# Kernel tuning notes

Hardware: AMD Instinct MI355X
Metric: run time of the kernel (lower is better)

## Reference

```python
import jax, jax.numpy as jnp
import numpy as np

N = 4000      # number_of_sensors
D_IN = 128    # input feature dim
D_OUT = 128   # output feature dim
E_DIM = 16    # node embedding dim
B = 8         # batch size


def setup_inputs() -> dict:
    key = jax.random.key(0)
    k_x, k_e1, k_e2, k_w = jax.random.split(key, 4)
    x = jax.random.normal(k_x, (B, N, D_IN), dtype=jnp.float32)
    E1 = jax.random.normal(k_e1, (N, E_DIM), dtype=jnp.float32)
    E2 = jax.random.normal(k_e2, (N, E_DIM), dtype=jnp.float32)
    W = jax.random.normal(k_w, (D_IN, D_OUT), dtype=jnp.float32) * (1.0 / np.sqrt(D_IN))
    b = jnp.zeros((D_OUT,), dtype=jnp.float32)
    return {"x": x, "E1": E1, "E2": E2, "W": W, "b": b}


def reference(x, E1, E2, W, b):
    # Adaptive adjacency from node embeddings: A = softmax(relu(E1 @ E2^T), axis=-1)
    logits = jax.nn.relu(jnp.einsum('nd,md->nm', E1, E2))  # [N, N]
    adj = jax.nn.softmax(logits, axis=-1)                  # row-normalized adjacency
    # Graph aggregation then feature transform: relu(A @ X @ W + b)
    agg = jnp.einsum('nm,bmf->bnf', adj, x)                # [B, N, D_IN]
    out = jax.nn.relu(jnp.einsum('bnf,fo->bno', agg, W) + b)  # [B, N, D_OUT]
    return out
```

## Files before the change

kernel.cpp:

```cpp
#include <hip/hip_runtime.h>
#include <hip/hip_bf16.h>

#define NSEN 4000
#define NP   4096
#define DIN  128
#define DOUT 128
#define EDIM 16
#define BATCH 8

typedef __attribute__((ext_vector_type(8))) short bf16x8;
typedef __attribute__((ext_vector_type(4))) float f32x4;

__device__ __forceinline__ unsigned short f2bf(float f) {
  unsigned int u = __float_as_uint(f);
  unsigned int r = (u + 0x7FFFu + ((u >> 16) & 1u)) >> 16;
  return (unsigned short)r;
}
__device__ __forceinline__ float bf2f(unsigned short s) {
  unsigned int u = ((unsigned int)s) << 16;
  return __uint_as_float(u);
}

__device__ __forceinline__ void gl_lds16(const void* g, void* l) {
  __builtin_amdgcn_global_load_lds((const __attribute__((address_space(1))) void*)g,
                                   (__attribute__((address_space(3))) void*)l, 16, 0, 0);
}

__global__ __launch_bounds__(512) void k_prep(const float* __restrict__ E1,
                                              const float* __restrict__ E2,
                                              const float* __restrict__ W,
                                              const float* __restrict__ x,
                                              unsigned short* __restrict__ adjp,
                                              float* __restrict__ rinv,
                                              unsigned short* __restrict__ Wt,
                                              unsigned short* __restrict__ xpt) {
  __shared__ float rsum[8][16];
  __shared__ unsigned short xtile[2][64][72];
  const int bx = blockIdx.x;
  const int tid = threadIdx.x;

  if (bx == 250) {
    for (int i = tid; i < DIN * DOUT; i += 512) {
      int o = i >> 7, f = i & 127;
      Wt[i] = f2bf(W[(size_t)f * DOUT + o]);
    }
    return;
  }
  if (bx > 250) {
    const int tile = (bx - 251) * 2 + (tid >> 8);
    const int t = tid & 255;
    const int sub = tid >> 8;
    const int m0 = (tile & 63) * 64;
    const int f0 = ((tile >> 6) & 1) * 64;
    const int b  = tile >> 7;
    const int f4 = t & 15, mrow = t >> 4;
#pragma unroll
    for (int rep = 0; rep < 4; rep++) {
      int ml = mrow + rep * 16;
      int m = m0 + ml;
      float4 v = make_float4(0.f, 0.f, 0.f, 0.f);
      if (m < NSEN) v = *(const float4*)&x[((size_t)b * NSEN + m) * DIN + f0 + f4 * 4];
      xtile[sub][f4*4+0][ml] = f2bf(v.x);
      xtile[sub][f4*4+1][ml] = f2bf(v.y);
      xtile[sub][f4*4+2][ml] = f2bf(v.z);
      xtile[sub][f4*4+3][ml] = f2bf(v.w);
    }
    __syncthreads();
    const int seg = t & 7, fl0 = t >> 3;
#pragma unroll
    for (int it = 0; it < 2; it++) {
      int fl = fl0 + it * 32;
      int j = b * DIN + f0 + fl;
      uint4 v = *(const uint4*)&xtile[sub][fl][seg * 8];
      *(uint4*)&xpt[(size_t)j * NP + m0 + seg * 8] = v;
    }
    return;
  }

  const int lane = tid & 63, wv = tid >> 6;
  const int lr = lane & 15, lq = lane >> 4;
  const int n0 = bx * 16;

  float a[8];
  {
    const float* e1p = &E1[(size_t)(n0 + lr) * EDIM + (lq & 1) * 8];
    *(float4*)&a[0] = *(const float4*)e1p;
    *(float4*)&a[4] = *(const float4*)(e1p + 4);
  }
  bf16x8 af1, af2;
#pragma unroll
  for (int j = 0; j < 8; j++) {
    unsigned short hs = f2bf(a[j]);
    af1[j] = (short)hs;
    float lo = a[j] - bf2f(hs);
    af2[j] = (lq < 2) ? (short)f2bf(lo) : (short)0;
  }

  float rs[4] = {0.f, 0.f, 0.f, 0.f};
  for (int t = wv; t < NSEN / 16; t += 8) {
    const int m = t * 16 + lr;
    float bv[8];
    const float* e2p = &E2[(size_t)m * EDIM + (lq & 1) * 8];
    *(float4*)&bv[0] = *(const float4*)e2p;
    *(float4*)&bv[4] = *(const float4*)(e2p + 4);
    bf16x8 bfrag;
#pragma unroll
    for (int j = 0; j < 8; j++) {
      unsigned short hs = f2bf(bv[j]);
      if (lq < 2) bfrag[j] = (short)hs;
      else        bfrag[j] = (short)f2bf(bv[j] - bf2f(hs));
    }
    f32x4 c = (f32x4){0.f, 0.f, 0.f, 0.f};
    c = __builtin_amdgcn_mfma_f32_16x16x32_bf16(af1, bfrag, c, 0, 0, 0);
    c = __builtin_amdgcn_mfma_f32_16x16x32_bf16(af2, bfrag, c, 0, 0, 0);
#pragma unroll
    for (int i = 0; i < 4; i++) {
      float p = __expf(fmaxf(c[i], 0.f));
      rs[i] += p;
      adjp[(size_t)(n0 + lq * 4 + i) * NP + t * 16 + lr] = f2bf(p);
    }
  }
  for (int i = tid; i < 16 * (NP - NSEN); i += 512) {
    int r = i / (NP - NSEN), c = i % (NP - NSEN);
    adjp[(size_t)(n0 + r) * NP + NSEN + c] = 0;
  }
#pragma unroll
  for (int i = 0; i < 4; i++) {
    rs[i] += __shfl_xor(rs[i], 1, 64);
    rs[i] += __shfl_xor(rs[i], 2, 64);
    rs[i] += __shfl_xor(rs[i], 4, 64);
    rs[i] += __shfl_xor(rs[i], 8, 64);
  }
  if (lr == 0) {
#pragma unroll
    for (int i = 0; i < 4; i++) rsum[wv][lq * 4 + i] = rs[i];
  }
  __syncthreads();
  if (tid < 16) {
    float s = 0.f;
#pragma unroll
    for (int w = 0; w < 8; w++) s += rsum[w][tid];
    rinv[n0 + tid] = 1.0f / s;
  }
}

__global__ __launch_bounds__(256, 2) void k_gemm1(const unsigned short* __restrict__ A,
                                                  const unsigned short* __restrict__ Bt,
                                                  unsigned short* __restrict__ part) {
  __shared__ __align__(16) unsigned short smem[32768];
  const int tid = threadIdx.x;
  const int lane = tid & 63, wv = tid >> 6;
  const int wr = wv >> 1, wc = wv & 1;
  const int lr = lane & 15, lq = lane >> 4;
  const int gx = blockIdx.x;
  const int m0 = (gx >> 1) * 128;
  const int kb0 = (gx & 1) * 2048;
  const int b  = blockIdx.y;
  const int c0 = b * 128;
  unsigned short* tA0 = smem;
  unsigned short* tB0 = smem + 16384;

  f32x4 acc[4][4];
#pragma unroll
  for (int p = 0; p < 4; p++)
#pragma unroll
    for (int q = 0; q < 4; q++) acc[p][q] = (f32x4){0.f, 0.f, 0.f, 0.f};

#define STAGE(bufi, kb)                                                              \
  {                                                                                  \
    _Pragma("unroll")                                                                \
    for (int s = 0; s < 4; s++) {                                                    \
      int idx = s * 256 + tid;                                                       \
      int row = idx >> 3;                                                            \
      int kc = ((idx & 7) ^ (row & 7)) << 3;                                         \
      gl_lds16(&A[(size_t)(m0 + row) * NP + (kb) + kc], &tA0[(bufi)*8192 + idx*8]);  \
      gl_lds16(&Bt[(size_t)(c0 + row) * NP + (kb) + kc], &tB0[(bufi)*8192 + idx*8]); \
    }                                                                                \
  }

  STAGE(0, kb0);

  for (int it = 0; it < 32; ++it) {
    const int cur = it & 1;
    if (it < 31) {
      STAGE(cur ^ 1, kb0 + (it + 1) * 64);
      asm volatile("s_waitcnt vmcnt(8)" ::: "memory");
    } else {
      asm volatile("s_waitcnt vmcnt(0)" ::: "memory");
    }
    __builtin_amdgcn_s_barrier();

    bf16x8 af0[4], bf0[4], af1[4], bf1[4];
    {
      const int koff0 = (lq * 8) ^ ((lr & 7) << 3);
#pragma unroll
      for (int p = 0; p < 4; p++)
        af0[p] = *(const bf16x8*)&tA0[cur * 8192 + (wr * 64 + p * 16 + lr) * 64 + koff0];
#pragma unroll
      for (int q = 0; q < 4; q++)
        bf0[q] = *(const bf16x8*)&tB0[cur * 8192 + (wc * 64 + q * 16 + lr) * 64 + koff0];
    }
    __builtin_amdgcn_sched_barrier(0);
    {
      const int koff1 = (32 + lq * 8) ^ ((lr & 7) << 3);
#pragma unroll
      for (int p = 0; p < 4; p++)
        af1[p] = *(const bf16x8*)&tA0[cur * 8192 + (wr * 64 + p * 16 + lr) * 64 + koff1];
#pragma unroll
      for (int q = 0; q < 4; q++)
        bf1[q] = *(const bf16x8*)&tB0[cur * 8192 + (wc * 64 + q * 16 + lr) * 64 + koff1];
    }
    asm volatile("s_waitcnt lgkmcnt(8)" ::: "memory");
    __builtin_amdgcn_sched_barrier(0);
    __builtin_amdgcn_s_setprio(1);
#pragma unroll
    for (int p = 0; p < 4; p++)
#pragma unroll
      for (int q = 0; q < 4; q++)
        acc[p][q] = __builtin_amdgcn_mfma_f32_16x16x32_bf16(af0[p], bf0[q], acc[p][q], 0, 0, 0);
    asm volatile("s_waitcnt lgkmcnt(0)" ::: "memory");
    __builtin_amdgcn_sched_barrier(0);
#pragma unroll
    for (int p = 0; p < 4; p++)
#pragma unroll
      for (int q = 0; q < 4; q++)
        acc[p][q] = __builtin_amdgcn_mfma_f32_16x16x32_bf16(af1[p], bf1[q], acc[p][q], 0, 0, 0);
    __builtin_amdgcn_s_setprio(0);
    __builtin_amdgcn_s_barrier();
  }
#undef STAGE

  const int kh = gx & 1;
  unsigned short* pdst = part + ((size_t)(kh * BATCH + b) * NP + m0) * DIN;
#pragma unroll
  for (int p = 0; p < 4; p++)
#pragma unroll
    for (int q = 0; q < 4; q++) {
      const int col = wc * 64 + q * 16 + lr;
#pragma unroll
      for (int i = 0; i < 4; i++) {
        const int row = wr * 64 + p * 16 + lq * 4 + i;
        pdst[row * DIN + col] = f2bf(acc[p][q][i]);
      }
    }
}

__global__ __launch_bounds__(256, 2) void k_fin(const unsigned short* __restrict__ part,
                                                const unsigned short* __restrict__ Wt,
                                                const float* __restrict__ rinv,
                                                const float* __restrict__ bias,
                                                float* __restrict__ out) {
  __shared__ __align__(16) unsigned short eps[64 * 136];
  const int tid = threadIdx.x;
  const int lane = tid & 63, wv = tid >> 6;
  const int wr = wv >> 1, wc = wv & 1;
  const int lr = lane & 15, lq = lane >> 4;
  const int m0 = blockIdx.x * 64;
  const int b = blockIdx.y;
  const size_t base = ((size_t)b * NP + m0) * DIN;
  const size_t khoff = (size_t)BATCH * NP * DIN;

  bf16x8 wf[4][4];
#pragma unroll
  for (int q = 0; q < 4; q++)
#pragma unroll
    for (int ks = 0; ks < 4; ks++)
      wf[q][ks] = *(const bf16x8*)&Wt[(size_t)(wc * 64 + q * 16 + lr) * DIN + ks * 32 + lq * 8];

#pragma unroll
  for (int s = 0; s < 4; s++) {
    int c = s * 256 + tid;
    int row = c >> 4, col = (c & 15) * 8;
    bf16x8 p0 = *(const bf16x8*)&part[base + row * DIN + col];
    bf16x8 p1 = *(const bf16x8*)&part[khoff + base + row * DIN + col];
    float rv = rinv[m0 + row];
    unsigned short tmp[8];
#pragma unroll
    for (int j = 0; j < 8; j++)
      tmp[j] = f2bf((bf2f((unsigned short)p0[j]) + bf2f((unsigned short)p1[j])) * rv);
    *(bf16x8*)&eps[row * 136 + col] = *(bf16x8*)tmp;
  }
  __syncthreads();

  f32x4 acc2[2][4];
#pragma unroll
  for (int p = 0; p < 2; p++)
#pragma unroll
    for (int q = 0; q < 4; q++) acc2[p][q] = (f32x4){0.f, 0.f, 0.f, 0.f};

#pragma unroll
  for (int ks = 0; ks < 4; ks++) {
    bf16x8 a2[2];
#pragma unroll
    for (int p = 0; p < 2; p++)
      a2[p] = *(const bf16x8*)&eps[(wr * 32 + p * 16 + lr) * 136 + ks * 32 + lq * 8];
#pragma unroll
    for (int p = 0; p < 2; p++)
#pragma unroll
      for (int q = 0; q < 4; q++)
        acc2[p][q] = __builtin_amdgcn_mfma_f32_16x16x32_bf16(a2[p], wf[q][ks], acc2[p][q], 0, 0, 0);
  }

#pragma unroll
  for (int p = 0; p < 2; p++)
#pragma unroll
    for (int q = 0; q < 4; q++) {
      const int o = wc * 64 + q * 16 + lr;
      const float bb = bias[o];
#pragma unroll
      for (int i = 0; i < 4; i++) {
        const int n = m0 + wr * 32 + p * 16 + lq * 4 + i;
        if (n < NSEN)
          out[((size_t)b * NSEN + n) * DOUT + o] = fmaxf(acc2[p][q][i] + bb, 0.f);
      }
    }
}

extern "C" void kernel_launch(void* const* d_in, const int* in_sizes, int n_in,
                              void* d_out, int out_size, void* d_ws, size_t ws_size,
                              hipStream_t stream) {
  const float* x    = (const float*)d_in[0];
  const float* E1   = (const float*)d_in[1];
  const float* E2   = (const float*)d_in[2];
  const float* W    = (const float*)d_in[3];
  const float* bias = (const float*)d_in[4];
  float* out = (float*)d_out;

  char* ws = (char*)d_ws;
  unsigned short* adjp = (unsigned short*)(ws);
  unsigned short* xpt  = (unsigned short*)(ws + 33554432);
  unsigned short* wt   = (unsigned short*)(ws + 33554432 + 8388608);
  float*          rinv = (float*)(ws + 33554432 + 8388608 + 32768);
  unsigned short* part = (unsigned short*)(ws + 33554432 + 8388608 + 32768 + 16384);

  k_prep<<<dim3(763), dim3(512), 0, stream>>>(E1, E2, W, x, adjp, rinv, wt, xpt);
  k_gemm1<<<dim3(64, BATCH), dim3(256), 0, stream>>>(adjp, xpt, part);
  k_fin<<<dim3(63, BATCH), dim3(256), 0, stream>>>(part, wt, rinv, bias, out);
}
```

Measured before the change: 72.17 us.

## Reassociate A·X·W as A·(X·W) and fold W GEMM into prep

The feature transform X·W is now computed first, inside the prep kernel, using MFMA and written transposed in bf16, replacing the plain x transpose and W transpose. The big adjacency GEMM then multiplies by Y=XW, so the final kernel becomes a simple elementwise pass: sum the two split-K partials, scale by the inverse row sum, add bias and apply relu. This removes the second GEMM and its LDS staging from the tail kernel. In exchange the prep blocks do more compute and each reloads and converts W from fp32 with strided reads, and rounding Y to bf16 before aggregation changes the numerics slightly.

```diff
diff --git a/kernel.cpp b/kernel.cpp
--- a/kernel.cpp
+++ b/kernel.cpp
@@ -32,53 +32,66 @@
                                               const float* __restrict__ x,
                                               unsigned short* __restrict__ adjp,
                                               float* __restrict__ rinv,
-                                              unsigned short* __restrict__ Wt,
-                                              unsigned short* __restrict__ xpt) {
+                                              unsigned short* __restrict__ yt) {
   __shared__ float rsum[8][16];
-  __shared__ unsigned short xtile[2][64][72];
   const int bx = blockIdx.x;
   const int tid = threadIdx.x;
-
-  if (bx == 250) {
-    for (int i = tid; i < DIN * DOUT; i += 512) {
-      int o = i >> 7, f = i & 127;
-      Wt[i] = f2bf(W[(size_t)f * DOUT + o]);
-    }
-    return;
-  }
-  if (bx > 250) {
-    const int tile = (bx - 251) * 2 + (tid >> 8);
-    const int t = tid & 255;
-    const int sub = tid >> 8;
-    const int m0 = (tile & 63) * 64;
-    const int f0 = ((tile >> 6) & 1) * 64;
-    const int b  = tile >> 7;
-    const int f4 = t & 15, mrow = t >> 4;
-#pragma unroll
-    for (int rep = 0; rep < 4; rep++) {
-      int ml = mrow + rep * 16;
-      int m = m0 + ml;
-      float4 v = make_float4(0.f, 0.f, 0.f, 0.f);
-      if (m < NSEN) v = *(const float4*)&x[((size_t)b * NSEN + m) * DIN + f0 + f4 * 4];
-      xtile[sub][f4*4+0][ml] = f2bf(v.x);
-      xtile[sub][f4*4+1][ml] = f2bf(v.y);
-      xtile[sub][f4*4+2][ml] = f2bf(v.z);
-      xtile[sub][f4*4+3][ml] = f2bf(v.w);
-    }
-    __syncthreads();
-    const int seg = t & 7, fl0 = t >> 3;
-#pragma unroll
-    for (int it = 0; it < 2; it++) {
-      int fl = fl0 + it * 32;
-      int j = b * DIN + f0 + fl;
-      uint4 v = *(const uint4*)&xtile[sub][fl][seg * 8];
-      *(uint4*)&xpt[(size_t)j * NP + m0 + seg * 8] = v;
-    }
-    return;
-  }
-
   const int lane = tid & 63, wv = tid >> 6;
   const int lr = lane & 15, lq = lane >> 4;
+
+  if (bx >= 250) {
+    const int yi = bx - 250;
+    const int b  = yi >> 6;
+    const int mt = yi & 63;
+    const int m0 = mt * 64;
+    const int mh = wv >> 2;
+    const int os = wv & 3;
+    bf16x8 af[2][4];
+#pragma unroll
+    for (int ot = 0; ot < 2; ot++) {
+      const int ob = os * 32 + ot * 16 + lr;
+#pragma unroll
+      for (int ks = 0; ks < 4; ks++)
+#pragma unroll
+        for (int j = 0; j < 8; j++)
+          af[ot][ks][j] = (short)f2bf(W[(size_t)(ks * 32 + lq * 8 + j) * DOUT + ob]);
+    }
+#pragma unroll
+    for (int mtile = 0; mtile < 2; mtile++) {
+      const int mb = m0 + mh * 32 + mtile * 16;
+      const int m = mb + lr;
+      bf16x8 bx8[4];
+      if (m < NSEN) {
+        const float* xp = &x[((size_t)b * NSEN + m) * DIN + lq * 8];
+#pragma unroll
+        for (int ks = 0; ks < 4; ks++) {
+          float4 v0 = *(const float4*)(xp + ks * 32);
+          float4 v1 = *(const float4*)(xp + ks * 32 + 4);
+          bx8[ks][0] = (short)f2bf(v0.x); bx8[ks][1] = (short)f2bf(v0.y);
+          bx8[ks][2] = (short)f2bf(v0.z); bx8[ks][3] = (short)f2bf(v0.w);
+          bx8[ks][4] = (short)f2bf(v1.x); bx8[ks][5] = (short)f2bf(v1.y);
+          bx8[ks][6] = (short)f2bf(v1.z); bx8[ks][7] = (short)f2bf(v1.w);
+        }
+      } else {
+#pragma unroll
+        for (int ks = 0; ks < 4; ks++)
+#pragma unroll
+          for (int j = 0; j < 8; j++) bx8[ks][j] = 0;
+      }
+#pragma unroll
+      for (int ot = 0; ot < 2; ot++) {
+        f32x4 c = (f32x4){0.f, 0.f, 0.f, 0.f};
+#pragma unroll
+        for (int ks = 0; ks < 4; ks++)
+          c = __builtin_amdgcn_mfma_f32_16x16x32_bf16(af[ot][ks], bx8[ks], c, 0, 0, 0);
+#pragma unroll
+        for (int i = 0; i < 4; i++)
+          yt[(size_t)(b * 128 + os * 32 + ot * 16 + lq * 4 + i) * NP + mb + lr] = f2bf(c[i]);
+      }
+    }
+    return;
+  }
+
   const int n0 = bx * 16;
 
   float a[8];
@@ -245,75 +258,32 @@
     }
 }
 
-__global__ __launch_bounds__(256, 2) void k_fin(const unsigned short* __restrict__ part,
-                                                const unsigned short* __restrict__ Wt,
-                                                const float* __restrict__ rinv,
-                                                const float* __restrict__ bias,
-                                                float* __restrict__ out) {
-  __shared__ __align__(16) unsigned short eps[64 * 136];
+__global__ __launch_bounds__(256) void k_fin(const unsigned short* __restrict__ part,
+                                             const float* __restrict__ rinv,
+                                             const float* __restrict__ bias,
+                                             float* __restrict__ out) {
   const int tid = threadIdx.x;
-  const int lane = tid & 63, wv = tid >> 6;
-  const int wr = wv >> 1, wc = wv & 1;
-  const int lr = lane & 15, lq = lane >> 4;
-  const int m0 = blockIdx.x * 64;
-  const int b = blockIdx.y;
-  const size_t base = ((size_t)b * NP + m0) * DIN;
+  const int nl = tid >> 4;
+  const int ch = tid & 15;
+  const int n  = blockIdx.x * 16 + nl;
+  const int b  = blockIdx.y;
+  const size_t base = ((size_t)b * NP + n) * DIN + ch * 8;
   const size_t khoff = (size_t)BATCH * NP * DIN;
 
-  bf16x8 wf[4][4];
-#pragma unroll
-  for (int q = 0; q < 4; q++)
-#pragma unroll
-    for (int ks = 0; ks < 4; ks++)
-      wf[q][ks] = *(const bf16x8*)&Wt[(size_t)(wc * 64 + q * 16 + lr) * DIN + ks * 32 + lq * 8];
-
-#pragma unroll
-  for (int s = 0; s < 4; s++) {
-    int c = s * 256 + tid;
-    int row = c >> 4, col = (c & 15) * 8;
-    bf16x8 p0 = *(const bf16x8*)&part[base + row * DIN + col];
-    bf16x8 p1 = *(const bf16x8*)&part[khoff + base + row * DIN + col];
-    float rv = rinv[m0 + row];
-    unsigned short tmp[8];
-#pragma unroll
-    for (int j = 0; j < 8; j++)
-      tmp[j] = f2bf((bf2f((unsigned short)p0[j]) + bf2f((unsigned short)p1[j])) * rv);
-    *(bf16x8*)&eps[row * 136 + col] = *(bf16x8*)tmp;
-  }
-  __syncthreads();
-
-  f32x4 acc2[2][4];
-#pragma unroll
-  for (int p = 0; p < 2; p++)
-#pragma unroll
-    for (int q = 0; q < 4; q++) acc2[p][q] = (f32x4){0.f, 0.f, 0.f, 0.f};
-
-#pragma unroll
-  for (int ks = 0; ks < 4; ks++) {
-    bf16x8 a2[2];
-#pragma unroll
-    for (int p = 0; p < 2; p++)
-      a2[p] = *(const bf16x8*)&eps[(wr * 32 + p * 16 + lr) * 136 + ks * 32 + lq * 8];
-#pragma unroll
-    for (int p = 0; p < 2; p++)
-#pragma unroll
-      for (int q = 0; q < 4; q++)
-        acc2[p][q] = __builtin_amdgcn_mfma_f32_16x16x32_bf16(a2[p], wf[q][ks], acc2[p][q], 0, 0, 0);
-  }
-
-#pragma unroll
-  for (int p = 0; p < 2; p++)
-#pragma unroll
-    for (int q = 0; q < 4; q++) {
-      const int o = wc * 64 + q * 16 + lr;
-      const float bb = bias[o];
-#pragma unroll
-      for (int i = 0; i < 4; i++) {
-        const int n = m0 + wr * 32 + p * 16 + lq * 4 + i;
-        if (n < NSEN)
-          out[((size_t)b * NSEN + n) * DOUT + o] = fmaxf(acc2[p][q][i] + bb, 0.f);
-      }
-    }
+  bf16x8 p0 = *(const bf16x8*)&part[base];
+  bf16x8 p1 = *(const bf16x8*)&part[khoff + base];
+  const float rv = rinv[n];
+  float4 bb0 = *(const float4*)&bias[ch * 8];
+  float4 bb1 = *(const float4*)&bias[ch * 8 + 4];
+  float r[8];
+#pragma unroll
+  for (int j = 0; j < 8; j++) {
+    float bbj = (j < 4) ? ((const float*)&bb0)[j] : ((const float*)&bb1)[j - 4];
+    r[j] = fmaxf((bf2f((unsigned short)p0[j]) + bf2f((unsigned short)p1[j])) * rv + bbj, 0.f);
+  }
+  float* op = &out[((size_t)b * NSEN + n) * DOUT + ch * 8];
+  *(float4*)op       = make_float4(r[0], r[1], r[2], r[3]);
+  *(float4*)(op + 4) = make_float4(r[4], r[5], r[6], r[7]);
 }
 
 extern "C" void kernel_launch(void* const* d_in, const int* in_sizes, int n_in,
@@ -328,12 +298,11 @@
 
   char* ws = (char*)d_ws;
   unsigned short* adjp = (unsigned short*)(ws);
-  unsigned short* xpt  = (unsigned short*)(ws + 33554432);
-  unsigned short* wt   = (unsigned short*)(ws + 33554432 + 8388608);
-  float*          rinv = (float*)(ws + 33554432 + 8388608 + 32768);
-  unsigned short* part = (unsigned short*)(ws + 33554432 + 8388608 + 32768 + 16384);
-
-  k_prep<<<dim3(763), dim3(512), 0, stream>>>(E1, E2, W, x, adjp, rinv, wt, xpt);
-  k_gemm1<<<dim3(64, BATCH), dim3(256), 0, stream>>>(adjp, xpt, part);
-  k_fin<<<dim3(63, BATCH), dim3(256), 0, stream>>>(part, wt, rinv, bias, out);
-}
+  unsigned short* yt   = (unsigned short*)(ws + 33554432);
+  float*          rinv = (float*)(ws + 33554432 + 8388608);
+  unsigned short* part = (unsigned short*)(ws + 33554432 + 8388608 + 16384);
+
+  k_prep<<<dim3(762), dim3(512), 0, stream>>>(E1, E2, W, x, adjp, rinv, yt);
+  k_gemm1<<<dim3(64, BATCH), dim3(256), 0, stream>>>(adjp, yt, part);
+  k_fin<<<dim3(250, BATCH), dim3(256), 0, stream>>>(part, rinv, bias, out);
+}
```

After: 77.84 us. 7.9% more time.
